# Kernel optimization log

Measured on AMD Instinct MI355X. Metric: run time of the kernel, lower is better.

Reference implementation:

```python
import jax, jax.numpy as jnp
import numpy as np

H = 8
LAM = 0.01
NEG_INF = -1e9


def setup_inputs() -> dict:
    key = jax.random.key(0)
    ks = jax.random.split(key, 14)
    B, L, D = 256, 200, 256
    IN, HID = 64, 128
    f = jax.random.normal
    return {
        "x": f(ks[0], (B, L, D), jnp.float32),
        "user_g_emb": f(ks[1], (B, IN), jnp.float32),
        "fc1_w": f(ks[2], (IN, HID), jnp.float32) * (1.0 / np.sqrt(IN)),
        "fc1_b": f(ks[3], (HID,), jnp.float32) * 0.01,
        "fc2_w": f(ks[4], (HID, D * D), jnp.float32) * (1.0 / np.sqrt(HID)),
        "fc2_b": f(ks[5], (D * D,), jnp.float32) * 0.01,
        "base_w": f(ks[6], (D, D), jnp.float32) * (1.0 / np.sqrt(D)),
        "b_q": f(ks[7], (D,), jnp.float32) * 0.01,
        "Wk": f(ks[8], (D, D), jnp.float32) * (1.0 / np.sqrt(D)),
        "bk": f(ks[9], (D,), jnp.float32) * 0.01,
        "Wv": f(ks[10], (D, D), jnp.float32) * (1.0 / np.sqrt(D)),
        "bv": f(ks[11], (D,), jnp.float32) * 0.01,
        "Wo": f(ks[12], (D, D), jnp.float32) * (1.0 / np.sqrt(D)),
        "bo": f(ks[13], (D,), jnp.float32) * 0.01,
    }


def reference(x, user_g_emb, fc1_w, fc1_b, fc2_w, fc2_b, base_w, b_q,
              Wk, bk, Wv, bv, Wo, bo):
    B, L, D = x.shape
    dk = D // H
    # MetaNetwork: hypernetwork generating per-sample weight [B, D, D]
    h1 = jax.nn.sigmoid(user_g_emb @ fc1_w + fc1_b)          # [B, HID]
    fc_w = (h1 @ fc2_w + fc2_b).reshape(B, D, D)             # [B, D, D]
    # LinearForMeta_sc: scaling modulation + batched GEMM for query proj
    w1 = LAM * fc_w + base_w                                 # [B, D, D]
    q = jnp.einsum('bld,bde->ble', x, w1) + b_q              # [B, L, D]
    k = x @ Wk + bk                                          # [B, L, D]
    v = x @ Wv + bv                                          # [B, L, D]
    # split heads -> [B, H, L, dk]
    q = q.reshape(B, L, H, dk).transpose(0, 2, 1, 3)
    k = k.reshape(B, L, H, dk).transpose(0, 2, 1, 3)
    v = v.reshape(B, L, H, dk).transpose(0, 2, 1, 3)
    scores = jnp.einsum('bhld,bhmd->bhlm', q, k) / np.sqrt(dk)
    causal = jnp.tril(jnp.ones((L, L), dtype=bool))          # mask==0 -> -1e9
    scores = jnp.where(causal, scores, NEG_INF)
    p = jax.nn.softmax(scores, axis=-1)                      # [B, H, L, L]
    o = jnp.einsum('bhlm,bhmd->bhld', p, v)                  # [B, H, L, dk]
    o = o.transpose(0, 2, 1, 3).reshape(B, L, D)
    return o @ Wo + bo
```

## Files before the change

kernel.cpp:

```cpp
#include <hip/hip_runtime.h>

#define B_   256
#define L_   200
#define D_   256
#define H_   8
#define DK_  32
#define IN_  64
#define HID_ 128
#define LAM_ 0.01f

using f32x4 = __attribute__((ext_vector_type(4))) float;
using bf16x8 = __attribute__((ext_vector_type(8))) short;

__device__ inline unsigned short bf16_rn(float f) {
  unsigned int u = __float_as_uint(f);
  return (unsigned short)((u + 0x7fffu + ((u >> 16) & 1u)) >> 16);
}

__device__ inline f32x4 mfma16(f32x4 c, bf16x8 a, bf16x8 b) {
  return __builtin_amdgcn_mfma_f32_16x16x32_bf16(a, b, c, 0, 0, 0);
}

__global__ __launch_bounds__(256) void cast_x_k(const float* __restrict__ x,
                                                unsigned short* __restrict__ xb) {
  long i = (long)blockIdx.x * 256 + threadIdx.x;
  const float4* px = (const float4*)x;
  float4 a = px[2 * i], b = px[2 * i + 1];
  unsigned int w0 = bf16_rn(a.x) | ((unsigned int)bf16_rn(a.y) << 16);
  unsigned int w1 = bf16_rn(a.z) | ((unsigned int)bf16_rn(a.w) << 16);
  unsigned int w2 = bf16_rn(b.x) | ((unsigned int)bf16_rn(b.y) << 16);
  unsigned int w3 = bf16_rn(b.z) | ((unsigned int)bf16_rn(b.w) << 16);
  *(uint4*)(xb + 8 * i) = make_uint4(w0, w1, w2, w3);
}

__global__ void hyper_h1(const float* __restrict__ ue, const float* __restrict__ fc1w,
                         const float* __restrict__ fc1b, float* __restrict__ h1t) {
  int b = blockIdx.x, j = threadIdx.x;
  __shared__ float us[IN_];
  if (j < IN_) us[j] = ue[b * IN_ + j];
  __syncthreads();
  float acc = fc1b[j];
#pragma unroll
  for (int i = 0; i < IN_; ++i) acc = fmaf(us[i], fc1w[i * HID_ + j], acc);
  h1t[j * B_ + b] = 1.f / (1.f + __expf(-acc));
}

__global__ void prep_wt(const float* __restrict__ Wk, const float* __restrict__ Wv,
                        const float* __restrict__ Wo, unsigned short* __restrict__ wkT,
                        unsigned short* __restrict__ wvT, unsigned short* __restrict__ woT) {
  const float* W = blockIdx.y == 0 ? Wk : (blockIdx.y == 1 ? Wv : Wo);
  unsigned short* O = blockIdx.y == 0 ? wkT : (blockIdx.y == 1 ? wvT : woT);
  int n = blockIdx.x, k = threadIdx.x;
  O[n * D_ + k] = bf16_rn(W[k * D_ + n]);
}

__global__ __launch_bounds__(256) void meta_w1(const float* __restrict__ h1t,
                                               const float* __restrict__ fc2w,
                                               const float* __restrict__ fc2b,
                                               const float* __restrict__ basew,
                                               unsigned short* __restrict__ w1) {
  int d = blockIdx.x, b0 = blockIdx.y * 32, e = threadIdx.x;
  float acc[32];
#pragma unroll
  for (int bb = 0; bb < 32; ++bb) acc[bb] = 0.f;
  const float* fw = fc2w + d * D_ + e;
  for (int j = 0; j < HID_; ++j) {
    float wv = fw[(long)j * (D_ * D_)];
    const float* hp = h1t + j * B_ + b0;
#pragma unroll
    for (int bb = 0; bb < 32; ++bb) acc[bb] = fmaf(hp[bb], wv, acc[bb]);
  }
  float add = LAM_ * fc2b[d * D_ + e] + basew[d * D_ + e];
#pragma unroll
  for (int bb = 0; bb < 32; ++bb)
    w1[(long)(b0 + bb) * (D_ * D_) + d * D_ + e] = bf16_rn(LAM_ * acc[bb] + add);
}

__global__ __launch_bounds__(256) void transpose_w1(const unsigned short* __restrict__ w1,
                                                    unsigned short* __restrict__ w1t) {
  __shared__ unsigned short t[32][36];
  long b = blockIdx.y;
  int d0 = (blockIdx.x >> 3) * 32, e0 = (blockIdx.x & 7) * 32;
  int r = threadIdx.x >> 3, c4 = (threadIdx.x & 7) * 4;
  const unsigned short* src = w1 + b * (D_ * D_);
  uint2 vv = *(const uint2*)(src + (d0 + r) * D_ + e0 + c4);
  *(uint2*)(&t[r][c4]) = vv;
  __syncthreads();
  unsigned short o0 = t[c4 + 0][r], o1 = t[c4 + 1][r], o2 = t[c4 + 2][r], o3 = t[c4 + 3][r];
  unsigned int lo = o0 | ((unsigned int)o1 << 16), hi = o2 | ((unsigned int)o3 << 16);
  *(uint2*)(w1t + b * (D_ * D_) + (e0 + r) * D_ + d0 + c4) = make_uint2(lo, hi);
}

template <int OUT_BF16>
__global__ __launch_bounds__(256) void gemm_bt(const unsigned short* __restrict__ A,
                                               const unsigned short* __restrict__ Wt,
                                               const float* __restrict__ bias,
                                               void* __restrict__ Cout, int Mvalid,
                                               long bsA, long bsW, long bsC) {
  __shared__ unsigned short ldsA[64][40];
  __shared__ unsigned short ldsB[64][40];
  int b = blockIdx.z;
  int row0 = blockIdx.x * 64, n0 = blockIdx.y * 64;
  int tid = threadIdx.x, lane = tid & 63, w = tid >> 6;
  int wr = w >> 1, wc = w & 1, c = lane & 15, g = lane >> 4;
  const unsigned short* Ab = A + (long)b * bsA;
  const unsigned short* Wb = Wt + (long)b * bsW;
  int sr = tid >> 2, sk = (tid & 3) * 8;
  long arow = row0 + sr;
  if (arow >= Mvalid) arow = Mvalid - 1;
  f32x4 zero = {0.f, 0.f, 0.f, 0.f};
  f32x4 acc[2][2];
#pragma unroll
  for (int mi = 0; mi < 2; ++mi)
#pragma unroll
    for (int ni = 0; ni < 2; ++ni) acc[mi][ni] = zero;

  for (int kt = 0; kt < 8; ++kt) {
    int k0 = kt * 32;
    uint4 av = *(const uint4*)(Ab + arow * D_ + k0 + sk);
    uint4 bv = *(const uint4*)(Wb + (long)(n0 + sr) * D_ + k0 + sk);
    __syncthreads();
    *(uint4*)(&ldsA[sr][sk]) = av;
    *(uint4*)(&ldsB[sr][sk]) = bv;
    __syncthreads();
    bf16x8 af[2], bfr[2];
#pragma unroll
    for (int mi = 0; mi < 2; ++mi) af[mi] = *(const bf16x8*)(&ldsA[wr * 32 + mi * 16 + c][g * 8]);
#pragma unroll
    for (int ni = 0; ni < 2; ++ni) bfr[ni] = *(const bf16x8*)(&ldsB[wc * 32 + ni * 16 + c][g * 8]);
#pragma unroll
    for (int mi = 0; mi < 2; ++mi)
#pragma unroll
      for (int ni = 0; ni < 2; ++ni) acc[mi][ni] = mfma16(acc[mi][ni], af[mi], bfr[ni]);
  }
#pragma unroll
  for (int mi = 0; mi < 2; ++mi)
#pragma unroll
    for (int ni = 0; ni < 2; ++ni) {
      int col = n0 + wc * 32 + ni * 16 + c;
      float bi = bias[col];
#pragma unroll
      for (int j = 0; j < 4; ++j) {
        int row = row0 + wr * 32 + mi * 16 + g * 4 + j;
        if (row < Mvalid) {
          float val = acc[mi][ni][j] + bi;
          long off = (long)b * bsC + (long)row * D_ + col;
          if (OUT_BF16)
            ((unsigned short*)Cout)[off] = bf16_rn(val);
          else
            ((float*)Cout)[off] = val;
        }
      }
    }
}

__global__ __launch_bounds__(256) void attn_k(const unsigned short* __restrict__ q,
                                              const unsigned short* __restrict__ k,
                                              const unsigned short* __restrict__ v,
                                              unsigned short* __restrict__ o) {
  __shared__ unsigned short ldsK[224][40];
  __shared__ unsigned short ldsVT[32][232];
  __shared__ unsigned short ldsP[64][232];
  int b = blockIdx.z, h = blockIdx.y, q0 = blockIdx.x * 64;
  int tid = threadIdx.x, lane = tid & 63, w = tid >> 6, c = lane & 15, g = lane >> 4;
  long base = ((long)b * L_) * D_ + h * DK_;

  for (int idx = tid; idx < 224 * 4; idx += 256) {
    int m = idx >> 2, pp = idx & 3;
    int mc = m < L_ ? m : L_ - 1;
    uint4 kv = *(const uint4*)(k + base + (long)mc * D_ + pp * 8);
    *(uint4*)(&ldsK[m][pp * 8]) = kv;
    uint4 vv = *(const uint4*)(v + base + (long)mc * D_ + pp * 8);
    const unsigned short* vs = (const unsigned short*)&vv;
#pragma unroll
    for (int dd = 0; dd < 8; ++dd) ldsVT[pp * 8 + dd][m] = vs[dd];
  }
  int ql = q0 + w * 16 + c;
  if (ql >= L_) ql = L_ - 1;
  bf16x8 qf = *(const bf16x8*)(q + base + (long)ql * D_ + g * 8);
  __syncthreads();

  f32x4 zero = {0.f, 0.f, 0.f, 0.f};
  f32x4 s[14];
#pragma unroll
  for (int mf = 0; mf < 14; ++mf) {
    bf16x8 kf = *(const bf16x8*)(&ldsK[mf * 16 + c][g * 8]);
    s[mf] = mfma16(zero, qf, kf);
  }
  const float scale = 0.17677669529663687f;
  int lg = q0 + w * 16 + g * 4;
#pragma unroll
  for (int mf = 0; mf < 14; ++mf) {
    int m = mf * 16 + c;
#pragma unroll
    for (int j = 0; j < 4; ++j) {
      bool val = (m <= lg + j) && (m < L_);
      s[mf][j] = val ? s[mf][j] * scale : -1e9f;
    }
  }
  float mx[4], sm[4];
#pragma unroll
  for (int j = 0; j < 4; ++j) {
    float m0 = s[0][j];
#pragma unroll
    for (int mf = 1; mf < 14; ++mf) m0 = fmaxf(m0, s[mf][j]);
    m0 = fmaxf(m0, __shfl_xor(m0, 1));
    m0 = fmaxf(m0, __shfl_xor(m0, 2));
    m0 = fmaxf(m0, __shfl_xor(m0, 4));
    m0 = fmaxf(m0, __shfl_xor(m0, 8));
    mx[j] = m0;
  }
#pragma unroll
  for (int j = 0; j < 4; ++j) {
    float ss = 0.f;
#pragma unroll
    for (int mf = 0; mf < 14; ++mf) {
      float p = __expf(s[mf][j] - mx[j]);
      s[mf][j] = p;
      ss += p;
    }
    ss += __shfl_xor(ss, 1);
    ss += __shfl_xor(ss, 2);
    ss += __shfl_xor(ss, 4);
    ss += __shfl_xor(ss, 8);
    sm[j] = ss;
  }
#pragma unroll
  for (int mf = 0; mf < 14; ++mf)
#pragma unroll
    for (int j = 0; j < 4; ++j) ldsP[w * 16 + g * 4 + j][mf * 16 + c] = bf16_rn(s[mf][j]);
  __syncthreads();

  f32x4 oa[2];
  oa[0] = zero;
  oa[1] = zero;
#pragma unroll
  for (int kb = 0; kb < 7; ++kb) {
    bf16x8 pf = *(const bf16x8*)(&ldsP[w * 16 + c][kb * 32 + g * 8]);
#pragma unroll
    for (int nf = 0; nf < 2; ++nf) {
      bf16x8 vf = *(const bf16x8*)(&ldsVT[nf * 16 + c][kb * 32 + g * 8]);
      oa[nf] = mfma16(oa[nf], pf, vf);
    }
  }
  float inv[4];
#pragma unroll
  for (int j = 0; j < 4; ++j) inv[j] = 1.f / sm[j];
#pragma unroll
  for (int nf = 0; nf < 2; ++nf)
#pragma unroll
    for (int j = 0; j < 4; ++j) {
      int l = q0 + w * 16 + g * 4 + j;
      if (l < L_) o[base + (long)l * D_ + nf * 16 + c] = bf16_rn(oa[nf][j] * inv[j]);
    }
}

extern "C" void kernel_launch(void* const* d_in, const int* in_sizes, int n_in,
                              void* d_out, int out_size, void* d_ws, size_t ws_size,
                              hipStream_t stream) {
  const float* x = (const float*)d_in[0];
  const float* ue = (const float*)d_in[1];
  const float* fc1w = (const float*)d_in[2];
  const float* fc1b = (const float*)d_in[3];
  const float* fc2w = (const float*)d_in[4];
  const float* fc2b = (const float*)d_in[5];
  const float* bw = (const float*)d_in[6];
  const float* bq = (const float*)d_in[7];
  const float* Wk = (const float*)d_in[8];
  const float* bk = (const float*)d_in[9];
  const float* Wv = (const float*)d_in[10];
  const float* bv = (const float*)d_in[11];
  const float* Wo = (const float*)d_in[12];
  const float* bo = (const float*)d_in[13];

  char* ws = (char*)d_ws;
  unsigned short* xb = (unsigned short*)(ws + 0);
  unsigned short* qb = (unsigned short*)(ws + 26214400);
  unsigned short* w1 = (unsigned short*)(ws + 52428800);
  unsigned short* w1t = (unsigned short*)(ws + 85983232);
  float* h1t = (float*)(ws + 119537664);
  unsigned short* wkT = (unsigned short*)(ws + 119668736);
  unsigned short* wvT = (unsigned short*)(ws + 119799808);
  unsigned short* woT = (unsigned short*)(ws + 119930880);
  unsigned short* kb_ = w1;
  unsigned short* vb = w1t;
  unsigned short* ob = xb;

  cast_x_k<<<6400, 256, 0, stream>>>(x, xb);
  hyper_h1<<<256, 128, 0, stream>>>(ue, fc1w, fc1b, h1t);
  prep_wt<<<dim3(256, 3), 256, 0, stream>>>(Wk, Wv, Wo, wkT, wvT, woT);
  meta_w1<<<dim3(256, 8), 256, 0, stream>>>(h1t, fc2w, fc2b, bw, w1);
  transpose_w1<<<dim3(64, 256), 256, 0, stream>>>(w1, w1t);
  gemm_bt<1><<<dim3(4, 4, 256), 256, 0, stream>>>(xb, w1t, bq, qb, L_, (long)L_ * D_,
                                                  (long)D_ * D_, (long)L_ * D_);
  gemm_bt<1><<<dim3(800, 4, 1), 256, 0, stream>>>(xb, wkT, bk, kb_, B_ * L_, 0L, 0L, 0L);
  gemm_bt<1><<<dim3(800, 4, 1), 256, 0, stream>>>(xb, wvT, bv, vb, B_ * L_, 0L, 0L, 0L);
  attn_k<<<dim3(4, H_, B_), 256, 0, stream>>>(qb, kb_, vb, ob);
  gemm_bt<0><<<dim3(800, 4, 1), 256, 0, stream>>>(ob, woT, bo, d_out, B_ * L_, 0L, 0L, 0L);
}
```

Baseline: 436.6 us.

## Compute hypernetwork weights via MFMA GEMM and restructure projections and attention

Replaces the scalar fp32 meta_w1 kernel and separate transpose with a pre-transposed bf16 fc2 weight plus an MFMA GEMM that writes the transposed per-sample weight directly. All projection GEMMs move to a new 64x256 tile kernel with XCD-aware block mapping. The V projection emits a transposed layout so attention no longer transposes V in LDS. Attention skips fully masked causal key tiles and reuses LDS between K and P. Costs: bf16 rounding of h1 and fc2 weights changes numerics, and the larger tiles use more registers, which may lower occupancy.

Measured after the change: 558.7 us. 27.9% more time.

```diff
diff --git a/kernel.cpp b/kernel.cpp
--- a/kernel.cpp
+++ b/kernel.cpp
@@ -34,7 +34,7 @@
 }
 
 __global__ void hyper_h1(const float* __restrict__ ue, const float* __restrict__ fc1w,
-                         const float* __restrict__ fc1b, float* __restrict__ h1t) {
+                         const float* __restrict__ fc1b, unsigned short* __restrict__ h1b) {
   int b = blockIdx.x, j = threadIdx.x;
   __shared__ float us[IN_];
   if (j < IN_) us[j] = ue[b * IN_ + j];
@@ -42,7 +42,7 @@
   float acc = fc1b[j];
 #pragma unroll
   for (int i = 0; i < IN_; ++i) acc = fmaf(us[i], fc1w[i * HID_ + j], acc);
-  h1t[j * B_ + b] = 1.f / (1.f + __expf(-acc));
+  h1b[b * HID_ + j] = bf16_rn(1.f / (1.f + __expf(-acc)));
 }
 
 __global__ void prep_wt(const float* __restrict__ Wk, const float* __restrict__ Wv,
@@ -54,126 +54,167 @@
   O[n * D_ + k] = bf16_rn(W[k * D_ + n]);
 }
 
-__global__ __launch_bounds__(256) void meta_w1(const float* __restrict__ h1t,
-                                               const float* __restrict__ fc2w,
-                                               const float* __restrict__ fc2b,
-                                               const float* __restrict__ basew,
-                                               unsigned short* __restrict__ w1) {
-  int d = blockIdx.x, b0 = blockIdx.y * 32, e = threadIdx.x;
-  float acc[32];
-#pragma unroll
-  for (int bb = 0; bb < 32; ++bb) acc[bb] = 0.f;
-  const float* fw = fc2w + d * D_ + e;
-  for (int j = 0; j < HID_; ++j) {
-    float wv = fw[(long)j * (D_ * D_)];
-    const float* hp = h1t + j * B_ + b0;
-#pragma unroll
-    for (int bb = 0; bb < 32; ++bb) acc[bb] = fmaf(hp[bb], wv, acc[bb]);
-  }
-  float add = LAM_ * fc2b[d * D_ + e] + basew[d * D_ + e];
-#pragma unroll
-  for (int bb = 0; bb < 32; ++bb)
-    w1[(long)(b0 + bb) * (D_ * D_) + d * D_ + e] = bf16_rn(LAM_ * acc[bb] + add);
-}
-
-__global__ __launch_bounds__(256) void transpose_w1(const unsigned short* __restrict__ w1,
-                                                    unsigned short* __restrict__ w1t) {
-  __shared__ unsigned short t[32][36];
-  long b = blockIdx.y;
-  int d0 = (blockIdx.x >> 3) * 32, e0 = (blockIdx.x & 7) * 32;
-  int r = threadIdx.x >> 3, c4 = (threadIdx.x & 7) * 4;
-  const unsigned short* src = w1 + b * (D_ * D_);
-  uint2 vv = *(const uint2*)(src + (d0 + r) * D_ + e0 + c4);
-  *(uint2*)(&t[r][c4]) = vv;
-  __syncthreads();
-  unsigned short o0 = t[c4 + 0][r], o1 = t[c4 + 1][r], o2 = t[c4 + 2][r], o3 = t[c4 + 3][r];
-  unsigned int lo = o0 | ((unsigned int)o1 << 16), hi = o2 | ((unsigned int)o3 << 16);
-  *(uint2*)(w1t + b * (D_ * D_) + (e0 + r) * D_ + d0 + c4) = make_uint2(lo, hi);
-}
-
-template <int OUT_BF16>
-__global__ __launch_bounds__(256) void gemm_bt(const unsigned short* __restrict__ A,
-                                               const unsigned short* __restrict__ Wt,
-                                               const float* __restrict__ bias,
-                                               void* __restrict__ Cout, int Mvalid,
-                                               long bsA, long bsW, long bsC) {
-  __shared__ unsigned short ldsA[64][40];
-  __shared__ unsigned short ldsB[64][40];
-  int b = blockIdx.z;
-  int row0 = blockIdx.x * 64, n0 = blockIdx.y * 64;
+__global__ __launch_bounds__(256) void prep_fc2(const float* __restrict__ fc2w,
+                                                const float* __restrict__ fc2b,
+                                                const float* __restrict__ basew,
+                                                unsigned short* __restrict__ fc2wT,
+                                                float* __restrict__ bias2) {
+  __shared__ float t[32][33];
+  int de0 = blockIdx.x * 32, j0 = blockIdx.y * 32;
+  int tid = threadIdx.x;
+  {
+    int jj = tid >> 3, dd4 = (tid & 7) * 4;
+    float4 v = *(const float4*)(fc2w + (long)(j0 + jj) * (D_ * D_) + de0 + dd4);
+    t[jj][dd4] = v.x; t[jj][dd4 + 1] = v.y; t[jj][dd4 + 2] = v.z; t[jj][dd4 + 3] = v.w;
+  }
+  __syncthreads();
+  int dd = tid >> 3, jj4 = (tid & 7) * 4;
+  int de = de0 + dd;
+  int n = (de & 255) * 256 + (de >> 8);
+  unsigned short r0 = bf16_rn(LAM_ * t[jj4 + 0][dd]);
+  unsigned short r1 = bf16_rn(LAM_ * t[jj4 + 1][dd]);
+  unsigned short r2 = bf16_rn(LAM_ * t[jj4 + 2][dd]);
+  unsigned short r3 = bf16_rn(LAM_ * t[jj4 + 3][dd]);
+  unsigned int lo = r0 | ((unsigned int)r1 << 16), hi = r2 | ((unsigned int)r3 << 16);
+  *(uint2*)(fc2wT + (long)n * HID_ + j0 + jj4) = make_uint2(lo, hi);
+  if (blockIdx.y == 0 && (tid & 7) == 0)
+    bias2[n] = LAM_ * fc2b[de] + basew[de];
+}
+
+template <int OUT_MODE, int KSTEPS>
+__global__ __launch_bounds__(256) void gemm64x256(
+    const unsigned short* __restrict__ A, const unsigned short* __restrict__ Wt,
+    const float* __restrict__ bias, void* __restrict__ Cout,
+    int Mvalid, int ldA, int ldW, int ldC,
+    long bsA, long bsW, long bsBias, long bsC, int nMt, int nB) {
+  __shared__ unsigned short ldsA[64 * 40];
+  __shared__ unsigned short ldsB[256 * 40];
+  int id = blockIdx.x;
+  int b, mt;
+  if (nB > 1) {
+    int xcd = id & 7, t = id >> 3;
+    b = (t / nMt) * 8 + xcd;
+    mt = t % nMt;
+  } else {
+    b = 0;
+    mt = id;
+  }
+  int row0 = mt * 64;
   int tid = threadIdx.x, lane = tid & 63, w = tid >> 6;
-  int wr = w >> 1, wc = w & 1, c = lane & 15, g = lane >> 4;
+  int c = lane & 15, g = lane >> 4;
   const unsigned short* Ab = A + (long)b * bsA;
   const unsigned short* Wb = Wt + (long)b * bsW;
   int sr = tid >> 2, sk = (tid & 3) * 8;
   long arow = row0 + sr;
   if (arow >= Mvalid) arow = Mvalid - 1;
-  f32x4 zero = {0.f, 0.f, 0.f, 0.f};
-  f32x4 acc[2][2];
-#pragma unroll
-  for (int mi = 0; mi < 2; ++mi)
-#pragma unroll
-    for (int ni = 0; ni < 2; ++ni) acc[mi][ni] = zero;
-
-  for (int kt = 0; kt < 8; ++kt) {
+  f32x4 acc[4][4];
+#pragma unroll
+  for (int mi = 0; mi < 4; ++mi)
+#pragma unroll
+    for (int ni = 0; ni < 4; ++ni) acc[mi][ni] = (f32x4){0.f, 0.f, 0.f, 0.f};
+
+  for (int kt = 0; kt < KSTEPS; ++kt) {
     int k0 = kt * 32;
-    uint4 av = *(const uint4*)(Ab + arow * D_ + k0 + sk);
-    uint4 bv = *(const uint4*)(Wb + (long)(n0 + sr) * D_ + k0 + sk);
+    uint4 av = *(const uint4*)(Ab + arow * ldA + k0 + sk);
+    uint4 bv[4];
+#pragma unroll
+    for (int i = 0; i < 4; ++i)
+      bv[i] = *(const uint4*)(Wb + (long)(sr + i * 64) * ldW + k0 + sk);
     __syncthreads();
-    *(uint4*)(&ldsA[sr][sk]) = av;
-    *(uint4*)(&ldsB[sr][sk]) = bv;
+    *(uint4*)(&ldsA[sr * 40 + sk]) = av;
+#pragma unroll
+    for (int i = 0; i < 4; ++i) *(uint4*)(&ldsB[(sr + i * 64) * 40 + sk]) = bv[i];
     __syncthreads();
-    bf16x8 af[2], bfr[2];
-#pragma unroll
-    for (int mi = 0; mi < 2; ++mi) af[mi] = *(const bf16x8*)(&ldsA[wr * 32 + mi * 16 + c][g * 8]);
-#pragma unroll
-    for (int ni = 0; ni < 2; ++ni) bfr[ni] = *(const bf16x8*)(&ldsB[wc * 32 + ni * 16 + c][g * 8]);
-#pragma unroll
-    for (int mi = 0; mi < 2; ++mi)
-#pragma unroll
-      for (int ni = 0; ni < 2; ++ni) acc[mi][ni] = mfma16(acc[mi][ni], af[mi], bfr[ni]);
-  }
-#pragma unroll
-  for (int mi = 0; mi < 2; ++mi)
-#pragma unroll
-    for (int ni = 0; ni < 2; ++ni) {
-      int col = n0 + wc * 32 + ni * 16 + c;
-      float bi = bias[col];
-#pragma unroll
-      for (int j = 0; j < 4; ++j) {
-        int row = row0 + wr * 32 + mi * 16 + g * 4 + j;
-        if (row < Mvalid) {
-          float val = acc[mi][ni][j] + bi;
-          long off = (long)b * bsC + (long)row * D_ + col;
-          if (OUT_BF16)
-            ((unsigned short*)Cout)[off] = bf16_rn(val);
-          else
-            ((float*)Cout)[off] = val;
+    bf16x8 af[4], bf[4];
+#pragma unroll
+    for (int mi = 0; mi < 4; ++mi) af[mi] = *(const bf16x8*)(&ldsA[(mi * 16 + c) * 40 + g * 8]);
+#pragma unroll
+    for (int ni = 0; ni < 4; ++ni)
+      bf[ni] = *(const bf16x8*)(&ldsB[(w * 64 + ni * 16 + c) * 40 + g * 8]);
+#pragma unroll
+    for (int mi = 0; mi < 4; ++mi)
+#pragma unroll
+      for (int ni = 0; ni < 4; ++ni) acc[mi][ni] = mfma16(acc[mi][ni], af[mi], bf[ni]);
+  }
+
+  if (OUT_MODE != 2) {
+#pragma unroll
+    for (int mi = 0; mi < 4; ++mi)
+#pragma unroll
+      for (int ni = 0; ni < 4; ++ni) {
+        int col = w * 64 + ni * 16 + c;
+        float bi = bias[b * bsBias + col];
+#pragma unroll
+        for (int j = 0; j < 4; ++j) {
+          int row = row0 + mi * 16 + g * 4 + j;
+          if (row < Mvalid) {
+            float val = acc[mi][ni][j] + bi;
+            long off = (long)b * bsC + (long)row * ldC + col;
+            if (OUT_MODE == 1)
+              ((unsigned short*)Cout)[off] = bf16_rn(val);
+            else
+              ((float*)Cout)[off] = val;
+          }
         }
       }
-    }
+  } else {
+    __syncthreads();
+#pragma unroll
+    for (int h = 0; h < 2; ++h) {
+#pragma unroll
+      for (int mi2 = 0; mi2 < 2; ++mi2) {
+        int mi = h * 2 + mi2;
+#pragma unroll
+        for (int ni = 0; ni < 4; ++ni) {
+          int col = w * 64 + ni * 16 + c;
+          float bi = bias[col];
+#pragma unroll
+          for (int j = 0; j < 4; ++j)
+            ldsB[col * 40 + mi2 * 16 + g * 4 + j] = bf16_rn(acc[mi][ni][j] + bi);
+        }
+      }
+      __syncthreads();
+      int m0 = row0 + h * 32;
+      if (m0 < 224) {
+        int col = tid;
+        unsigned short* dst = (unsigned short*)Cout + (long)b * bsC + (long)col * ldC + m0;
+        uint4 q0 = *(const uint4*)(&ldsB[col * 40 + 0]);
+        uint4 q1 = *(const uint4*)(&ldsB[col * 40 + 8]);
+        uint4 q2 = *(const uint4*)(&ldsB[col * 40 + 16]);
+        uint4 q3 = *(const uint4*)(&ldsB[col * 40 + 24]);
+        *(uint4*)(dst + 0) = q0;
+        *(uint4*)(dst + 8) = q1;
+        *(uint4*)(dst + 16) = q2;
+        *(uint4*)(dst + 24) = q3;
+      }
+      __syncthreads();
+    }
+  }
 }
 
 __global__ __launch_bounds__(256) void attn_k(const unsigned short* __restrict__ q,
                                               const unsigned short* __restrict__ k,
-                                              const unsigned short* __restrict__ v,
+                                              const unsigned short* __restrict__ vT,
                                               unsigned short* __restrict__ o) {
-  __shared__ unsigned short ldsK[224][40];
-  __shared__ unsigned short ldsVT[32][232];
-  __shared__ unsigned short ldsP[64][232];
+  __shared__ unsigned short smem[22272];
+  unsigned short* sKP = smem;
+  unsigned short* sV = smem + 14848;
   int b = blockIdx.z, h = blockIdx.y, q0 = blockIdx.x * 64;
   int tid = threadIdx.x, lane = tid & 63, w = tid >> 6, c = lane & 15, g = lane >> 4;
   long base = ((long)b * L_) * D_ + h * DK_;
-
-  for (int idx = tid; idx < 224 * 4; idx += 256) {
-    int m = idx >> 2, pp = idx & 3;
+  long vbase = ((long)b * D_ + h * DK_) * 224;
+
+  int nfr = min(13, (q0 + 64) >> 4);
+  int nkb = min(7, (q0 + 64) >> 5);
+
+  for (int idx = tid; idx < 896; idx += 256) {
+    int m = idx >> 2, dd = idx & 3;
     int mc = m < L_ ? m : L_ - 1;
-    uint4 kv = *(const uint4*)(k + base + (long)mc * D_ + pp * 8);
-    *(uint4*)(&ldsK[m][pp * 8]) = kv;
-    uint4 vv = *(const uint4*)(v + base + (long)mc * D_ + pp * 8);
-    const unsigned short* vs = (const unsigned short*)&vv;
-#pragma unroll
-    for (int dd = 0; dd < 8; ++dd) ldsVT[pp * 8 + dd][m] = vs[dd];
+    *(uint4*)(&sKP[m * 40 + dd * 8]) = *(const uint4*)(k + base + (long)mc * D_ + dd * 8);
+  }
+  for (int idx = tid; idx < 896; idx += 256) {
+    int d = idx / 28, mc8 = (idx % 28) * 8;
+    *(uint4*)(&sV[d * 232 + mc8]) = *(const uint4*)(vT + vbase + (long)d * 224 + mc8);
   }
   int ql = q0 + w * 16 + c;
   if (ql >= L_) ql = L_ - 1;
@@ -181,29 +222,32 @@
   __syncthreads();
 
   f32x4 zero = {0.f, 0.f, 0.f, 0.f};
-  f32x4 s[14];
-#pragma unroll
-  for (int mf = 0; mf < 14; ++mf) {
-    bf16x8 kf = *(const bf16x8*)(&ldsK[mf * 16 + c][g * 8]);
-    s[mf] = mfma16(zero, qf, kf);
-  }
+  f32x4 s[13];
+#pragma unroll
+  for (int mf = 0; mf < 13; ++mf)
+    if (mf < nfr) {
+      bf16x8 kf = *(const bf16x8*)(&sKP[(mf * 16 + c) * 40 + g * 8]);
+      s[mf] = mfma16(zero, qf, kf);
+    }
   const float scale = 0.17677669529663687f;
   int lg = q0 + w * 16 + g * 4;
 #pragma unroll
-  for (int mf = 0; mf < 14; ++mf) {
-    int m = mf * 16 + c;
-#pragma unroll
-    for (int j = 0; j < 4; ++j) {
-      bool val = (m <= lg + j) && (m < L_);
-      s[mf][j] = val ? s[mf][j] * scale : -1e9f;
-    }
-  }
-  float mx[4], sm[4];
+  for (int mf = 0; mf < 13; ++mf)
+    if (mf < nfr) {
+      int m = mf * 16 + c;
+#pragma unroll
+      for (int j = 0; j < 4; ++j) {
+        bool ok = (m <= lg + j) && (m < L_);
+        s[mf][j] = ok ? s[mf][j] * scale : -1e9f;
+      }
+    }
+  float mx[4], sm[4], inv[4];
 #pragma unroll
   for (int j = 0; j < 4; ++j) {
-    float m0 = s[0][j];
-#pragma unroll
-    for (int mf = 1; mf < 14; ++mf) m0 = fmaxf(m0, s[mf][j]);
+    float m0 = -1e9f;
+#pragma unroll
+    for (int mf = 0; mf < 13; ++mf)
+      if (mf < nfr) m0 = fmaxf(m0, s[mf][j]);
     m0 = fmaxf(m0, __shfl_xor(m0, 1));
     m0 = fmaxf(m0, __shfl_xor(m0, 2));
     m0 = fmaxf(m0, __shfl_xor(m0, 4));
@@ -214,38 +258,46 @@
   for (int j = 0; j < 4; ++j) {
     float ss = 0.f;
 #pragma unroll
-    for (int mf = 0; mf < 14; ++mf) {
-      float p = __expf(s[mf][j] - mx[j]);
-      s[mf][j] = p;
-      ss += p;
-    }
+    for (int mf = 0; mf < 13; ++mf)
+      if (mf < nfr) {
+        float p = __expf(s[mf][j] - mx[j]);
+        s[mf][j] = p;
+        ss += p;
+      }
     ss += __shfl_xor(ss, 1);
     ss += __shfl_xor(ss, 2);
     ss += __shfl_xor(ss, 4);
     ss += __shfl_xor(ss, 8);
     sm[j] = ss;
-  }
-#pragma unroll
-  for (int mf = 0; mf < 14; ++mf)
-#pragma unroll
-    for (int j = 0; j < 4; ++j) ldsP[w * 16 + g * 4 + j][mf * 16 + c] = bf16_rn(s[mf][j]);
+    inv[j] = 1.f / ss;
+  }
+  __syncthreads();
+  int row = w * 16 + g * 4;
+#pragma unroll
+  for (int mf = 0; mf < 14; ++mf) {
+    if (mf < nfr) {
+#pragma unroll
+      for (int j = 0; j < 4; ++j) sKP[(row + j) * 232 + mf * 16 + c] = bf16_rn(s[mf][j]);
+    } else if (mf < 2 * nkb) {
+#pragma unroll
+      for (int j = 0; j < 4; ++j) sKP[(row + j) * 232 + mf * 16 + c] = 0;
+    }
+  }
   __syncthreads();
 
   f32x4 oa[2];
   oa[0] = zero;
   oa[1] = zero;
 #pragma unroll
-  for (int kb = 0; kb < 7; ++kb) {
-    bf16x8 pf = *(const bf16x8*)(&ldsP[w * 16 + c][kb * 32 + g * 8]);
-#pragma unroll
-    for (int nf = 0; nf < 2; ++nf) {
-      bf16x8 vf = *(const bf16x8*)(&ldsVT[nf * 16 + c][kb * 32 + g * 8]);
-      oa[nf] = mfma16(oa[nf], pf, vf);
-    }
-  }
-  float inv[4];
-#pragma unroll
-  for (int j = 0; j < 4; ++j) inv[j] = 1.f / sm[j];
+  for (int kb = 0; kb < 7; ++kb)
+    if (kb < nkb) {
+      bf16x8 pf = *(const bf16x8*)(&sKP[(w * 16 + c) * 232 + kb * 32 + g * 8]);
+#pragma unroll
+      for (int nf = 0; nf < 2; ++nf) {
+        bf16x8 vf = *(const bf16x8*)(&sV[(nf * 16 + c) * 232 + kb * 32 + g * 8]);
+        oa[nf] = mfma16(oa[nf], pf, vf);
+      }
+    }
 #pragma unroll
   for (int nf = 0; nf < 2; ++nf)
 #pragma unroll
@@ -276,25 +328,32 @@
   char* ws = (char*)d_ws;
   unsigned short* xb = (unsigned short*)(ws + 0);
   unsigned short* qb = (unsigned short*)(ws + 26214400);
-  unsigned short* w1 = (unsigned short*)(ws + 52428800);
-  unsigned short* w1t = (unsigned short*)(ws + 85983232);
-  float* h1t = (float*)(ws + 119537664);
-  unsigned short* wkT = (unsigned short*)(ws + 119668736);
-  unsigned short* wvT = (unsigned short*)(ws + 119799808);
-  unsigned short* woT = (unsigned short*)(ws + 119930880);
-  unsigned short* kb_ = w1;
-  unsigned short* vb = w1t;
+  unsigned short* w1t = (unsigned short*)(ws + 52428800);
+  unsigned short* fc2wT = (unsigned short*)(ws + 85983232);
+  unsigned short* kb_ = (unsigned short*)(ws + 85983232);
+  char* sm = ws + 112197632;
+  unsigned short* h1b = (unsigned short*)(sm);
+  float* bias2 = (float*)(sm + 65536);
+  unsigned short* wkT = (unsigned short*)(sm + 327680);
+  unsigned short* wvT = (unsigned short*)(sm + 458752);
+  unsigned short* woT = (unsigned short*)(sm + 589824);
+  unsigned short* vT = w1t;
   unsigned short* ob = xb;
 
   cast_x_k<<<6400, 256, 0, stream>>>(x, xb);
-  hyper_h1<<<256, 128, 0, stream>>>(ue, fc1w, fc1b, h1t);
+  hyper_h1<<<256, 128, 0, stream>>>(ue, fc1w, fc1b, h1b);
   prep_wt<<<dim3(256, 3), 256, 0, stream>>>(Wk, Wv, Wo, wkT, wvT, woT);
-  meta_w1<<<dim3(256, 8), 256, 0, stream>>>(h1t, fc2w, fc2b, bw, w1);
-  transpose_w1<<<dim3(64, 256), 256, 0, stream>>>(w1, w1t);
-  gemm_bt<1><<<dim3(4, 4, 256), 256, 0, stream>>>(xb, w1t, bq, qb, L_, (long)L_ * D_,
-                                                  (long)D_ * D_, (long)L_ * D_);
-  gemm_bt<1><<<dim3(800, 4, 1), 256, 0, stream>>>(xb, wkT, bk, kb_, B_ * L_, 0L, 0L, 0L);
-  gemm_bt<1><<<dim3(800, 4, 1), 256, 0, stream>>>(xb, wvT, bv, vb, B_ * L_, 0L, 0L, 0L);
-  attn_k<<<dim3(4, H_, B_), 256, 0, stream>>>(qb, kb_, vb, ob);
-  gemm_bt<0><<<dim3(800, 4, 1), 256, 0, stream>>>(ob, woT, bo, d_out, B_ * L_, 0L, 0L, 0L);
-}
+  prep_fc2<<<dim3(2048, 4), 256, 0, stream>>>(fc2w, fc2b, bw, fc2wT, bias2);
+  gemm64x256<1, 4><<<1024, 256, 0, stream>>>(h1b, fc2wT, bias2, w1t, B_, HID_, HID_,
+                                             D_ * D_, 0L, 256L * HID_, 256L, 256L, 4, 256);
+  gemm64x256<1, 8><<<1024, 256, 0, stream>>>(xb, w1t, bq, qb, L_, D_, D_, D_,
+                                             (long)L_ * D_, (long)D_ * D_, 0L, (long)L_ * D_,
+                                             4, 256);
+  gemm64x256<1, 8><<<800, 256, 0, stream>>>(xb, wkT, bk, kb_, B_ * L_, D_, D_, D_,
+                                            0L, 0L, 0L, 0L, 800, 1);
+  gemm64x256<2, 8><<<1024, 256, 0, stream>>>(xb, wvT, bv, vT, L_, D_, D_, 224,
+                                             (long)L_ * D_, 0L, 0L, 256L * 224L, 4, 256);
+  attn_k<<<dim3(4, H_, B_), 256, 0, stream>>>(qb, kb_, vT, ob);
+  gemm64x256<0, 8><<<800, 256, 0, stream>>>(ob, woT, bo, d_out, B_ * L_, D_, D_, D_,
+                                            0L, 0L, 0L, 0L, 800, 1);
+}
```
